# Kernel tuning notes

Hardware: AMD Instinct MI355X
Metric: run time of the kernel (lower is better)

## Reference

```python
import jax, jax.numpy as jnp
import numpy as np

B, S, D = 4, 2048, 1024
H, DK, DV = 16, 64, 64


def setup_inputs() -> dict:
    key = jax.random.key(0)
    ks = jax.random.split(key, 12)
    scale = 1.0 / np.sqrt(D)
    queries = jax.random.normal(ks[0], (B, S, D), dtype=jnp.float32)
    keys_ = jax.random.normal(ks[1], (B, S, D), dtype=jnp.float32)
    values = jax.random.normal(ks[2], (B, S, D), dtype=jnp.float32)
    # binary additive mask (1 = masked out), broadcastable over batch and heads
    mask = jax.random.randint(ks[3], (1, 1, S, S), 0, 2).astype(jnp.float32)
    Wq = jax.random.normal(ks[4], (D, H * DK), dtype=jnp.float32) * scale
    bq = jnp.zeros((H * DK,), dtype=jnp.float32)
    Wk = jax.random.normal(ks[5], (D, H * DK), dtype=jnp.float32) * scale
    bk = jnp.zeros((H * DK,), dtype=jnp.float32)
    Wv = jax.random.normal(ks[6], (D, H * DV), dtype=jnp.float32) * scale
    bv = jnp.zeros((H * DV,), dtype=jnp.float32)
    Wo = jax.random.normal(ks[7], (H * DV, D), dtype=jnp.float32) * scale
    bo = jnp.zeros((D,), dtype=jnp.float32)
    return {"queries": queries, "keys": keys_, "values": values, "mask": mask,
            "Wq": Wq, "bq": bq, "Wk": Wk, "bk": bk, "Wv": Wv, "bv": bv,
            "Wo": Wo, "bo": bo}


def reference(queries, keys, values, mask, Wq, bq, Wk, bk, Wv, bv, Wo, bo):
    b = queries.shape[0]
    # projections + split heads: [B, S, H*Dh] -> [B, H, S, Dh]
    q = (queries @ Wq + bq).reshape(b, -1, H, DK).transpose(0, 2, 1, 3)
    k = (keys @ Wk + bk).reshape(b, -1, H, DK).transpose(0, 2, 1, 3)
    v = (values @ Wv + bv).reshape(b, -1, H, DV).transpose(0, 2, 1, 3)
    scores = jnp.einsum("bhqd,bhkd->bhqk", q, k) / jnp.sqrt(jnp.float32(DK))
    scores = scores + mask * (-1e9)
    attn = jax.nn.softmax(scores, axis=-1)
    ctx = jnp.einsum("bhqk,bhkd->bhqd", attn, v)  # [B, H, S, DV]
    ctx = ctx.transpose(0, 2, 1, 3).reshape(b, -1, H * DV)
    return ctx @ Wo + bo
```

## Files before the change

### kernel.cpp

```cpp
#include <hip/hip_runtime.h>
#include <cstdint>
#include <cstddef>

typedef __attribute__((ext_vector_type(8))) short bf16x8;
typedef __attribute__((ext_vector_type(4))) short bf16x4;
typedef __attribute__((ext_vector_type(4))) float f32x4;

__device__ __forceinline__ unsigned short f2bf(float f) {
    union { float f; unsigned int u; } v; v.f = f;
    unsigned int r = v.u + 0x7FFFu + ((v.u >> 16) & 1u);
    return (unsigned short)(r >> 16);
}
__device__ __forceinline__ unsigned int pk2(float a, float b) {
    return (unsigned int)f2bf(a) | ((unsigned int)f2bf(b) << 16);
}
__device__ __forceinline__ unsigned int pkfast(float a, float b) {
    unsigned int ua = __builtin_bit_cast(unsigned int, a) + 0x8000u;
    unsigned int ub = __builtin_bit_cast(unsigned int, b) + 0x8000u;
    return __builtin_amdgcn_perm(ub, ua, 0x07060302u);
}

typedef __attribute__((address_space(1))) void gvoid;
typedef __attribute__((address_space(3))) void svoid;
__device__ __forceinline__ void ld16_lds(const void* g, void* l) {
    __builtin_amdgcn_global_load_lds((gvoid*)g, (svoid*)l, 16, 0, 0);
}

#define QSCALE 0.1803368801111204f

__global__ __launch_bounds__(256)
void cvt_bf16(const float* __restrict__ A, const float* __restrict__ B,
              const float* __restrict__ C,
              unsigned short* __restrict__ oa, unsigned short* __restrict__ ob,
              unsigned short* __restrict__ oc)
{
    const float* src = (blockIdx.y == 0) ? A : (blockIdx.y == 1) ? B : C;
    unsigned short* dst = (blockIdx.y == 0) ? oa : (blockIdx.y == 1) ? ob : oc;
    const size_t i = ((size_t)blockIdx.x * 256 + threadIdx.x) * 8;
    float4 a = *(const float4*)(src + i);
    float4 b = *(const float4*)(src + i + 4);
    uint4 p;
    p.x = pk2(a.x, a.y); p.y = pk2(a.z, a.w);
    p.z = pk2(b.x, b.y); p.w = pk2(b.z, b.w);
    *(uint4*)(dst + i) = p;
}

__global__ __launch_bounds__(256)
void prep_weights(const float* __restrict__ W0, const float* __restrict__ W1,
                  const float* __restrict__ W2, const float* __restrict__ W3,
                  unsigned short* __restrict__ T0, unsigned short* __restrict__ T1,
                  unsigned short* __restrict__ T2, unsigned short* __restrict__ T3)
{
    __shared__ float t[32][33];
    const int z = blockIdx.z;
    const float* W = (z == 0) ? W0 : (z == 1) ? W1 : (z == 2) ? W2 : W3;
    unsigned short* Wt = (z == 0) ? T0 : (z == 1) ? T1 : (z == 2) ? T2 : T3;
    const int n0 = blockIdx.x * 32, k0 = blockIdx.y * 32;
    const int tx = threadIdx.x & 31, ty = threadIdx.x >> 5;
#pragma unroll
    for (int i = 0; i < 4; i++)
        t[ty + 8 * i][tx] = W[(size_t)(k0 + ty + 8 * i) * 1024 + n0 + tx];
    __syncthreads();
#pragma unroll
    for (int i = 0; i < 4; i++)
        Wt[(size_t)(n0 + ty + 8 * i) * 1024 + k0 + tx] = f2bf(t[tx][ty + 8 * i]);
}

__global__ __launch_bounds__(256)
void mask_pack(const float* __restrict__ m, unsigned char* __restrict__ bits)
{
    const size_t i = ((size_t)blockIdx.x * 256 + threadIdx.x) * 8;
    float4 a = *(const float4*)(m + i);
    float4 b = *(const float4*)(m + i + 4);
    unsigned c = 0;
    c |= (a.x != 0.f) ? 1u : 0u;
    c |= (a.y != 0.f) ? 2u : 0u;
    c |= (a.z != 0.f) ? 4u : 0u;
    c |= (a.w != 0.f) ? 8u : 0u;
    c |= (b.x != 0.f) ? 16u : 0u;
    c |= (b.y != 0.f) ? 32u : 0u;
    c |= (b.z != 0.f) ? 64u : 0u;
    c |= (b.w != 0.f) ? 128u : 0u;
    bits[i >> 3] = (unsigned char)c;
}

__global__ __launch_bounds__(256, 3)
void qkv_gemm(const unsigned short* __restrict__ A0,
              const unsigned short* __restrict__ W0,
              const float* __restrict__ bq, const float* __restrict__ bk,
              const float* __restrict__ bv,
              unsigned short* __restrict__ out0)
{
    __shared__ __align__(16) unsigned short sm[18432];

    const int z = blockIdx.z;
    const unsigned short* A  = A0 + ((size_t)z << 23);
    const unsigned short* Wt = W0 + ((size_t)z << 20);
    const float* bias = (z == 0) ? bq : (z == 1) ? bk : bv;
    unsigned short* ob = out0 + ((size_t)z << 23);

    const int tid = threadIdx.x, lane = tid & 63, wave = tid >> 6;
    const int quad = lane >> 4, l16 = lane & 15;
    const int wr = wave >> 1, wc = wave & 1;
    const int m0 = blockIdx.x * 128, n0 = blockIdx.y * 128;

    const char* Ab = (const char*)A  + (size_t)m0 * 2048;
    const char* Bb = (const char*)Wt + (size_t)n0 * 2048;
    const int sr0 = tid >> 2, sc0 = (tid & 3) << 4;

    f32x4 acc[4][4];
#pragma unroll
    for (int i = 0; i < 4; i++)
#pragma unroll
        for (int j = 0; j < 4; j++) acc[i][j] = (f32x4){0.f, 0.f, 0.f, 0.f};

    {
        char* Ad = (char*)sm;
        char* Bd = Ad + 8192;
        ld16_lds(Ab + (size_t)sr0 * 2048 + sc0,        Ad + tid * 16);
        ld16_lds(Ab + (size_t)(sr0 + 64) * 2048 + sc0, Ad + (256 + tid) * 16);
        ld16_lds(Bb + (size_t)sr0 * 2048 + sc0,        Bd + tid * 16);
        ld16_lds(Bb + (size_t)(sr0 + 64) * 2048 + sc0, Bd + (256 + tid) * 16);
    }

    for (int it = 0; it < 32; ++it) {
        const int cur = it & 1;
        __syncthreads();
        if (it < 31) {
            const int kb2 = (it + 1) * 64;
            char* Ad = (char*)(sm + (cur ^ 1) * 8192);
            char* Bd = Ad + 8192;
            ld16_lds(Ab + (size_t)sr0 * 2048 + kb2 + sc0,        Ad + tid * 16);
            ld16_lds(Ab + (size_t)(sr0 + 64) * 2048 + kb2 + sc0, Ad + (256 + tid) * 16);
            ld16_lds(Bb + (size_t)sr0 * 2048 + kb2 + sc0,        Bd + tid * 16);
            ld16_lds(Bb + (size_t)(sr0 + 64) * 2048 + kb2 + sc0, Bd + (256 + tid) * 16);
        }
        const unsigned short* As = sm + cur * 8192;
        const unsigned short* Bs = As + 4096;

        bf16x8 af[4], bfr[4];
#pragma unroll
        for (int mt = 0; mt < 4; mt++)
            af[mt] = *(const bf16x8*)&As[(wr * 64 + mt * 16 + l16) * 32 + quad * 8];
#pragma unroll
        for (int nt = 0; nt < 4; nt++)
            bfr[nt] = *(const bf16x8*)&Bs[(wc * 64 + nt * 16 + l16) * 32 + quad * 8];
#pragma unroll
        for (int mt = 0; mt < 4; mt++)
#pragma unroll
            for (int nt = 0; nt < 4; nt++)
                acc[mt][nt] = __builtin_amdgcn_mfma_f32_16x16x32_bf16(af[mt], bfr[nt], acc[mt][nt], 0, 0, 0);
    }

    float bvv[4];
#pragma unroll
    for (int nt = 0; nt < 4; nt++) bvv[nt] = bias[n0 + wc * 64 + nt * 16 + l16];

    if (z < 2) {
#pragma unroll
        for (int mt = 0; mt < 4; mt++) {
            const int m = m0 + wr * 64 + mt * 16 + quad * 4;
            const int b = m >> 11;
#pragma unroll
            for (int nt = 0; nt < 4; nt++) {
                const int n = n0 + wc * 64 + nt * 16 + l16;
                const int h = n >> 6, dk = n & 63;
#pragma unroll
                for (int r = 0; r < 4; r++) {
                    const int s = (m + r) & 2047;
                    float o = acc[mt][nt][r] + bvv[nt];
                    if (z == 0) o *= QSCALE;
                    ob[((size_t)((b << 4) + h) * 2048 + s) * 64 + dk] = f2bf(o);
                }
            }
        }
    } else {
        __syncthreads();
        unsigned short* T = sm + wave * (64 * 72);
#pragma unroll
        for (int mt = 0; mt < 4; mt++)
#pragma unroll
            for (int nt = 0; nt < 4; nt++)
#pragma unroll
                for (int r = 0; r < 4; r++)
                    T[(nt * 16 + l16) * 72 + mt * 16 + quad * 4 + r] = f2bf(acc[mt][nt][r] + bvv[nt]);
        __syncthreads();
#pragma unroll
        for (int i = 0; i < 8; i++) {
            const int nl = i * 8 + (lane >> 3);
            const int mc = lane & 7;
            uint4 v = *(const uint4*)&T[nl * 72 + mc * 8];
            const int n  = n0 + wc * 64 + nl;
            const int mg = m0 + wr * 64 + mc * 8;
            const int b = mg >> 11, s = mg & 2047;
            const int h = n >> 6, dv = n & 63;
            *(uint4*)&ob[((size_t)((b << 4) + h) * 64 + dv) * 2048 + s] = v;
        }
    }
}

__global__ __launch_bounds__(256, 3)
void gemm_final(const unsigned short* __restrict__ A,
                const unsigned short* __restrict__ Wt, const float* __restrict__ bias,
                float* __restrict__ of)
{
    __shared__ __align__(16) unsigned short sm[16384];

    const int tid = threadIdx.x, lane = tid & 63, wave = tid >> 6;
    const int quad = lane >> 4, l16 = lane & 15;
    const int wr = wave >> 1, wc = wave & 1;
    const int m0 = blockIdx.x * 128, n0 = blockIdx.y * 128;

    const char* Ab = (const char*)A  + (size_t)m0 * 2048;
    const char* Bb = (const char*)Wt + (size_t)n0 * 2048;
    const int sr0 = tid >> 2, sc0 = (tid & 3) << 4;

    f32x4 acc[4][4];
#pragma unroll
    for (int i = 0; i < 4; i++)
#pragma unroll
        for (int j = 0; j < 4; j++) acc[i][j] = (f32x4){0.f, 0.f, 0.f, 0.f};

    {
        char* Ad = (char*)sm;
        char* Bd = Ad + 8192;
        ld16_lds(Ab + (size_t)sr0 * 2048 + sc0,        Ad + tid * 16);
        ld16_lds(Ab + (size_t)(sr0 + 64) * 2048 + sc0, Ad + (256 + tid) * 16);
        ld16_lds(Bb + (size_t)sr0 * 2048 + sc0,        Bd + tid * 16);
        ld16_lds(Bb + (size_t)(sr0 + 64) * 2048 + sc0, Bd + (256 + tid) * 16);
    }

    for (int it = 0; it < 32; ++it) {
        const int cur = it & 1;
        __syncthreads();
        if (it < 31) {
            const int kb2 = (it + 1) * 64;
            char* Ad = (char*)(sm + (cur ^ 1) * 8192);
            char* Bd = Ad + 8192;
            ld16_lds(Ab + (size_t)sr0 * 2048 + kb2 + sc0,        Ad + tid * 16);
            ld16_lds(Ab + (size_t)(sr0 + 64) * 2048 + kb2 + sc0, Ad + (256 + tid) * 16);
            ld16_lds(Bb + (size_t)sr0 * 2048 + kb2 + sc0,        Bd + tid * 16);
            ld16_lds(Bb + (size_t)(sr0 + 64) * 2048 + kb2 + sc0, Bd + (256 + tid) * 16);
        }
        const unsigned short* As = sm + cur * 8192;
        const unsigned short* Bs = As + 4096;

        bf16x8 af[4], bfr[4];
#pragma unroll
        for (int mt = 0; mt < 4; mt++)
            af[mt] = *(const bf16x8*)&As[(wr * 64 + mt * 16 + l16) * 32 + quad * 8];
#pragma unroll
        for (int nt = 0; nt < 4; nt++)
            bfr[nt] = *(const bf16x8*)&Bs[(wc * 64 + nt * 16 + l16) * 32 + quad * 8];
#pragma unroll
        for (int mt = 0; mt < 4; mt++)
#pragma unroll
            for (int nt = 0; nt < 4; nt++)
                acc[mt][nt] = __builtin_amdgcn_mfma_f32_16x16x32_bf16(af[mt], bfr[nt], acc[mt][nt], 0, 0, 0);
    }

    float bvv[4];
#pragma unroll
    for (int nt = 0; nt < 4; nt++) bvv[nt] = bias[n0 + wc * 64 + nt * 16 + l16];
#pragma unroll
    for (int mt = 0; mt < 4; mt++) {
        const int m = m0 + wr * 64 + mt * 16 + quad * 4;
#pragma unroll
        for (int nt = 0; nt < 4; nt++) {
            const int n = n0 + wc * 64 + nt * 16 + l16;
#pragma unroll
            for (int r = 0; r < 4; r++)
                of[(size_t)(m + r) * 1024 + n] = acc[mt][nt][r] + bvv[nt];
        }
    }
}

__global__ __launch_bounds__(256, 4)
void attn_kernel(const unsigned short* __restrict__ q,
                 const unsigned short* __restrict__ k,
                 const unsigned short* __restrict__ vT,
                 const unsigned int* __restrict__ mbits,
                 unsigned short* __restrict__ ctx)
{
    __shared__ __align__(16) unsigned short Ks[2][64 * 64];
    __shared__ __align__(16) unsigned short Vs[2][64 * 64];

    const int tid = threadIdx.x, lane = tid & 63, wave = tid >> 6;
    const int quad = lane >> 4, l16 = lane & 15;
    const int sw = l16 & 7;
    const int bid = blockIdx.x;
    const int qblk = bid & 15, h = (bid >> 4) & 15, b = bid >> 8;

    const unsigned short* qb = q  + (size_t)(b * 16 + h) * 2048 * 64;
    const unsigned short* kb = k  + (size_t)(b * 16 + h) * 2048 * 64;
    const unsigned short* vb = vT + (size_t)(b * 16 + h) * 64 * 2048;

    const int c0 = tid, c1 = 256 + tid;
    const int r0 = c0 >> 3, gcc0 = (c0 & 7) ^ (r0 & 7);
    const int r1 = c1 >> 3, gcc1 = (c1 & 7) ^ (r1 & 7);

    int qrow[2];
    bf16x8 qf[2][2];
    f32x4 O0[4], O1[4];
    float l_i[2] = {0.f, 0.f};
#pragma unroll
    for (int g = 0; g < 2; g++) {
        qrow[g] = qblk * 128 + wave * 32 + g * 16 + l16;
        qf[g][0] = *(const bf16x8*)&qb[qrow[g] * 64 + quad * 8];
        qf[g][1] = *(const bf16x8*)&qb[qrow[g] * 64 + 32 + quad * 8];
    }
#pragma unroll
    for (int i = 0; i < 4; i++) { O0[i] = (f32x4){0.f,0.f,0.f,0.f}; O1[i] = (f32x4){0.f,0.f,0.f,0.f}; }
    const unsigned int* mrow0 = mbits + (size_t)qrow[0] * 64;
    const unsigned int* mrow1 = mbits + (size_t)qrow[1] * 64;

    {
        ld16_lds((const char*)kb + (size_t)r0 * 128 + gcc0 * 16, (char*)Ks[0] + c0 * 16);
        ld16_lds((const char*)kb + (size_t)r1 * 128 + gcc1 * 16, (char*)Ks[0] + c1 * 16);
        ld16_lds((const char*)vb + (size_t)r0 * 4096 + gcc0 * 16, (char*)Vs[0] + c0 * 16);
        ld16_lds((const char*)vb + (size_t)r1 * 4096 + gcc1 * 16, (char*)Vs[0] + c1 * 16);
    }
    uint2 mwc0 = *(const uint2*)&mrow0[0];
    uint2 mwc1 = *(const uint2*)&mrow1[0];

    for (int it = 0; it < 32; ++it) {
        const int kt = it << 6;
        const int cur = it & 1, nxt = cur ^ 1;
        __syncthreads();

        if (it < 31) {
            const char* kg = (const char*)kb + (size_t)(kt + 64) * 128;
            const char* vg = (const char*)vb + (size_t)(kt + 64) * 2;
            ld16_lds(kg + (size_t)r0 * 128 + gcc0 * 16, (char*)Ks[nxt] + c0 * 16);
            ld16_lds(kg + (size_t)r1 * 128 + gcc1 * 16, (char*)Ks[nxt] + c1 * 16);
            ld16_lds(vg + (size_t)r0 * 4096 + gcc0 * 16, (char*)Vs[nxt] + c0 * 16);
            ld16_lds(vg + (size_t)r1 * 4096 + gcc1 * 16, (char*)Vs[nxt] + c1 * 16);
        }
        const int mi = (it < 31) ? ((kt + 64) >> 5) : 0;
        uint2 mwn0 = *(const uint2*)&mrow0[mi];
        uint2 mwn1 = *(const uint2*)&mrow1[mi];

        const unsigned short* Kc = Ks[cur];
        const unsigned short* Vc = Vs[cur];

        f32x4 S0[4], S1[4];
#pragma unroll
        for (int mt = 0; mt < 4; mt++) {
            const unsigned short* kp = Kc + (mt * 16 + l16) * 64;
            bf16x8 ka0 = *(const bf16x8*)&kp[((quad    ) ^ sw) * 8];
            bf16x8 ka1 = *(const bf16x8*)&kp[((4 + quad) ^ sw) * 8];
            f32x4 z0 = (f32x4){0.f,0.f,0.f,0.f};
            f32x4 z1 = (f32x4){0.f,0.f,0.f,0.f};
            z0 = __builtin_amdgcn_mfma_f32_16x16x32_bf16(ka0, qf[0][0], z0, 0, 0, 0);
            S0[mt] = __builtin_amdgcn_mfma_f32_16x16x32_bf16(ka1, qf[0][1], z0, 0, 0, 0);
            z1 = __builtin_amdgcn_mfma_f32_16x16x32_bf16(ka0, qf[1][0], z1, 0, 0, 0);
            S1[mt] = __builtin_amdgcn_mfma_f32_16x16x32_bf16(ka1, qf[1][1], z1, 0, 0, 0);
        }
        float sum0 = 0.f, sum1 = 0.f;
        bf16x4 pf0[4], pf1[4];
#pragma unroll
        for (int mt = 0; mt < 4; mt++) {
            const unsigned int wm0 = ((mt & 2) ? mwc0.y : mwc0.x) >> (((mt & 1) << 4) + (quad << 2));
            const unsigned int wm1 = ((mt & 2) ? mwc1.y : mwc1.x) >> (((mt & 1) << 4) + (quad << 2));
#pragma unroll
            for (int r = 0; r < 4; r++) {
                float s0 = ((wm0 >> r) & 1u) ? -1e8f : S0[mt][r];
                float s1 = ((wm1 >> r) & 1u) ? -1e8f : S1[mt][r];
                s0 = __builtin_amdgcn_exp2f(s0);
                s1 = __builtin_amdgcn_exp2f(s1);
                S0[mt][r] = s0; sum0 += s0;
                S1[mt][r] = s1; sum1 += s1;
            }
            uint2 u0, u1;
            u0.x = pkfast(S0[mt][0], S0[mt][1]); u0.y = pkfast(S0[mt][2], S0[mt][3]);
            u1.x = pkfast(S1[mt][0], S1[mt][1]); u1.y = pkfast(S1[mt][2], S1[mt][3]);
            pf0[mt] = __builtin_bit_cast(bf16x4, u0);
            pf1[mt] = __builtin_bit_cast(bf16x4, u1);
        }
        l_i[0] += sum0; l_i[1] += sum1;

#pragma unroll
        for (int dvt = 0; dvt < 4; dvt++) {
            const unsigned short* vp = Vc + (dvt * 16 + l16) * 64;
#pragma unroll
            for (int mt = 0; mt < 4; mt++) {
                uint2 vv = *(const uint2*)&vp[((2 * mt + (quad >> 1)) ^ sw) * 8 + (quad & 1) * 4];
                bf16x4 va = __builtin_bit_cast(bf16x4, vv);
                O0[dvt] = __builtin_amdgcn_mfma_f32_16x16x16bf16_1k(va, pf0[mt], O0[dvt], 0, 0, 0);
                O1[dvt] = __builtin_amdgcn_mfma_f32_16x16x16bf16_1k(va, pf1[mt], O1[dvt], 0, 0, 0);
            }
        }
        mwc0 = mwn0; mwc1 = mwn1;
    }
#pragma unroll
    for (int g = 0; g < 2; g++) {
        float lsum = l_i[g];
        lsum += __shfl_xor(lsum, 16);
        lsum += __shfl_xor(lsum, 32);
        const float rl = __builtin_amdgcn_rcpf(lsum);
        const f32x4* O = g ? O1 : O0;
#pragma unroll
        for (int dvt = 0; dvt < 4; dvt++) {
            uint2 st;
            st.x = pk2(O[dvt][0] * rl, O[dvt][1] * rl);
            st.y = pk2(O[dvt][2] * rl, O[dvt][3] * rl);
            *(uint2*)&ctx[(size_t)(b * 2048 + qrow[g]) * 1024 + h * 64 + dvt * 16 + quad * 4] = st;
        }
    }
}

extern "C" void kernel_launch(void* const* d_in, const int* in_sizes, int n_in,
                              void* d_out, int out_size, void* d_ws, size_t ws_size,
                              hipStream_t stream)
{
    const float* Qin = (const float*)d_in[0];
    const float* Kin = (const float*)d_in[1];
    const float* Vin = (const float*)d_in[2];
    const float* Msk = (const float*)d_in[3];
    const float* Wq  = (const float*)d_in[4];
    const float* bq  = (const float*)d_in[5];
    const float* Wk  = (const float*)d_in[6];
    const float* bk  = (const float*)d_in[7];
    const float* Wv  = (const float*)d_in[8];
    const float* bv  = (const float*)d_in[9];
    const float* Wo  = (const float*)d_in[10];
    const float* bo  = (const float*)d_in[11];

    unsigned short* w = (unsigned short*)d_ws;
    unsigned short* wtq  = w;
    unsigned short* wtk  = w + (1u << 20);
    unsigned short* wtv  = w + 2u * (1u << 20);
    unsigned short* wto  = w + 3u * (1u << 20);
    unsigned short* qcv  = w + 4u * (1u << 20);
    unsigned short* kcv  = qcv + (1u << 23);
    unsigned short* vcv  = kcv + (1u << 23);
    unsigned short* qb   = vcv + (1u << 23);
    unsigned short* kb   = qb  + (1u << 23);
    unsigned short* vTb  = kb  + (1u << 23);
    unsigned short* ctxb = qcv;
    unsigned long long* mb = (unsigned long long*)(vTb + (1u << 23));

    prep_weights<<<dim3(32, 32, 4), 256, 0, stream>>>(Wq, Wk, Wv, Wo, wtq, wtk, wtv, wto);
    mask_pack<<<2048, 256, 0, stream>>>(Msk, (unsigned char*)mb);
    cvt_bf16<<<dim3(4096, 3), 256, 0, stream>>>(Qin, Kin, Vin, qcv, kcv, vcv);
    qkv_gemm<<<dim3(64, 8, 3), 256, 0, stream>>>(qcv, wtq, bq, bk, bv, qb);
    attn_kernel<<<1024, 256, 0, stream>>>(qb, kb, vTb, (const unsigned int*)mb, ctxb);
    gemm_final<<<dim3(64, 8), 256, 0, stream>>>(ctxb, wto, bo, (float*)d_out);
}
```

Baseline: 388.0 us.

## Merge preprocessing kernels, compute softmax denominator via MFMA, use native bf16 pack

The three preprocessing kernels (activation conversion, mask bit-packing, weight transpose) become one launch that dispatches on block index, removing two kernel launches. In the attention kernel the per-row softmax sum is now an MFMA against a ones vector instead of scalar adds plus cross-lane shuffles. The P packing uses the hardware bf16 pack instruction when available. The qkv_gemm launch bounds rise to 4 blocks per CU. The sum is now taken over the bf16-rounded probabilities, and the higher occupancy target may limit registers.

```diff
diff --git a/kernel.cpp b/kernel.cpp
--- a/kernel.cpp
+++ b/kernel.cpp
@@ -14,10 +14,15 @@
 __device__ __forceinline__ unsigned int pk2(float a, float b) {
     return (unsigned int)f2bf(a) | ((unsigned int)f2bf(b) << 16);
 }
-__device__ __forceinline__ unsigned int pkfast(float a, float b) {
+__device__ __forceinline__ unsigned int pkpair(float a, float b) {
+#if __has_builtin(__builtin_amdgcn_cvt_pk_bf16_f32)
+    auto r = __builtin_amdgcn_cvt_pk_bf16_f32(a, b);
+    return __builtin_bit_cast(unsigned int, r);
+#else
     unsigned int ua = __builtin_bit_cast(unsigned int, a) + 0x8000u;
     unsigned int ub = __builtin_bit_cast(unsigned int, b) + 0x8000u;
     return __builtin_amdgcn_perm(ub, ua, 0x07060302u);
+#endif
 }
 
 typedef __attribute__((address_space(1))) void gvoid;
@@ -29,62 +34,58 @@
 #define QSCALE 0.1803368801111204f
 
 __global__ __launch_bounds__(256)
-void cvt_bf16(const float* __restrict__ A, const float* __restrict__ B,
-              const float* __restrict__ C,
-              unsigned short* __restrict__ oa, unsigned short* __restrict__ ob,
-              unsigned short* __restrict__ oc)
-{
-    const float* src = (blockIdx.y == 0) ? A : (blockIdx.y == 1) ? B : C;
-    unsigned short* dst = (blockIdx.y == 0) ? oa : (blockIdx.y == 1) ? ob : oc;
-    const size_t i = ((size_t)blockIdx.x * 256 + threadIdx.x) * 8;
-    float4 a = *(const float4*)(src + i);
-    float4 b = *(const float4*)(src + i + 4);
-    uint4 p;
-    p.x = pk2(a.x, a.y); p.y = pk2(a.z, a.w);
-    p.z = pk2(b.x, b.y); p.w = pk2(b.z, b.w);
-    *(uint4*)(dst + i) = p;
-}
-
-__global__ __launch_bounds__(256)
-void prep_weights(const float* __restrict__ W0, const float* __restrict__ W1,
-                  const float* __restrict__ W2, const float* __restrict__ W3,
-                  unsigned short* __restrict__ T0, unsigned short* __restrict__ T1,
-                  unsigned short* __restrict__ T2, unsigned short* __restrict__ T3)
+void preprocess(const float* __restrict__ Qin, const float* __restrict__ Kin,
+                const float* __restrict__ Vin, const float* __restrict__ Msk,
+                const float* __restrict__ Wq, const float* __restrict__ Wk,
+                const float* __restrict__ Wv, const float* __restrict__ Wo,
+                unsigned short* __restrict__ acts, unsigned char* __restrict__ mbits,
+                unsigned short* __restrict__ wts)
 {
     __shared__ float t[32][33];
-    const int z = blockIdx.z;
-    const float* W = (z == 0) ? W0 : (z == 1) ? W1 : (z == 2) ? W2 : W3;
-    unsigned short* Wt = (z == 0) ? T0 : (z == 1) ? T1 : (z == 2) ? T2 : T3;
-    const int n0 = blockIdx.x * 32, k0 = blockIdx.y * 32;
-    const int tx = threadIdx.x & 31, ty = threadIdx.x >> 5;
-#pragma unroll
-    for (int i = 0; i < 4; i++)
-        t[ty + 8 * i][tx] = W[(size_t)(k0 + ty + 8 * i) * 1024 + n0 + tx];
-    __syncthreads();
-#pragma unroll
-    for (int i = 0; i < 4; i++)
-        Wt[(size_t)(n0 + ty + 8 * i) * 1024 + k0 + tx] = f2bf(t[tx][ty + 8 * i]);
-}
-
-__global__ __launch_bounds__(256)
-void mask_pack(const float* __restrict__ m, unsigned char* __restrict__ bits)
-{
-    const size_t i = ((size_t)blockIdx.x * 256 + threadIdx.x) * 8;
-    float4 a = *(const float4*)(m + i);
-    float4 b = *(const float4*)(m + i + 4);
-    unsigned c = 0;
-    c |= (a.x != 0.f) ? 1u : 0u;
-    c |= (a.y != 0.f) ? 2u : 0u;
-    c |= (a.z != 0.f) ? 4u : 0u;
-    c |= (a.w != 0.f) ? 8u : 0u;
-    c |= (b.x != 0.f) ? 16u : 0u;
-    c |= (b.y != 0.f) ? 32u : 0u;
-    c |= (b.z != 0.f) ? 64u : 0u;
-    c |= (b.w != 0.f) ? 128u : 0u;
-    bits[i >> 3] = (unsigned char)c;
-}
-
-__global__ __launch_bounds__(256, 3)
+    const int bx = blockIdx.x, tid = threadIdx.x;
+    if (bx < 12288) {
+        const int which = bx >> 12;
+        const float* src = (which == 0) ? Qin : (which == 1) ? Kin : Vin;
+        unsigned short* dst = acts + ((size_t)which << 23);
+        const size_t i = ((size_t)(bx & 4095) * 256 + tid) * 8;
+        float4 a = *(const float4*)(src + i);
+        float4 b = *(const float4*)(src + i + 4);
+        uint4 p;
+        p.x = pk2(a.x, a.y); p.y = pk2(a.z, a.w);
+        p.z = pk2(b.x, b.y); p.w = pk2(b.z, b.w);
+        *(uint4*)(dst + i) = p;
+    } else if (bx < 14336) {
+        const size_t i = ((size_t)(bx - 12288) * 256 + tid) * 8;
+        float4 a = *(const float4*)(Msk + i);
+        float4 b = *(const float4*)(Msk + i + 4);
+        unsigned c = 0;
+        c |= (a.x != 0.f) ? 1u : 0u;
+        c |= (a.y != 0.f) ? 2u : 0u;
+        c |= (a.z != 0.f) ? 4u : 0u;
+        c |= (a.w != 0.f) ? 8u : 0u;
+        c |= (b.x != 0.f) ? 16u : 0u;
+        c |= (b.y != 0.f) ? 32u : 0u;
+        c |= (b.z != 0.f) ? 64u : 0u;
+        c |= (b.w != 0.f) ? 128u : 0u;
+        mbits[i >> 3] = (unsigned char)c;
+    } else {
+        const int idx = bx - 14336;
+        const int z = idx >> 10, rem = idx & 1023;
+        const float* W = (z == 0) ? Wq : (z == 1) ? Wk : (z == 2) ? Wv : Wo;
+        unsigned short* Wt = wts + ((size_t)z << 20);
+        const int n0 = (rem & 31) << 5, k0 = (rem >> 5) << 5;
+        const int tx = tid & 31, ty = tid >> 5;
+#pragma unroll
+        for (int i = 0; i < 4; i++)
+            t[ty + 8 * i][tx] = W[(size_t)(k0 + ty + 8 * i) * 1024 + n0 + tx];
+        __syncthreads();
+#pragma unroll
+        for (int i = 0; i < 4; i++)
+            Wt[(size_t)(n0 + ty + 8 * i) * 1024 + k0 + tx] = f2bf(t[tx][ty + 8 * i]);
+    }
+}
+
+__global__ __launch_bounds__(256, 4)
 void qkv_gemm(const unsigned short* __restrict__ A0,
               const unsigned short* __restrict__ W0,
               const float* __restrict__ bq, const float* __restrict__ bk,
@@ -302,7 +303,8 @@
     int qrow[2];
     bf16x8 qf[2][2];
     f32x4 O0[4], O1[4];
-    float l_i[2] = {0.f, 0.f};
+    f32x4 lacc0 = (f32x4){0.f,0.f,0.f,0.f}, lacc1 = (f32x4){0.f,0.f,0.f,0.f};
+    const bf16x4 vones = (bf16x4){(short)0x3F80, (short)0x3F80, (short)0x3F80, (short)0x3F80};
 #pragma unroll
     for (int g = 0; g < 2; g++) {
         qrow[g] = qblk * 128 + wave * 32 + g * 16 + l16;
@@ -356,29 +358,28 @@
             z1 = __builtin_amdgcn_mfma_f32_16x16x32_bf16(ka0, qf[1][0], z1, 0, 0, 0);
             S1[mt] = __builtin_amdgcn_mfma_f32_16x16x32_bf16(ka1, qf[1][1], z1, 0, 0, 0);
         }
-        float sum0 = 0.f, sum1 = 0.f;
         bf16x4 pf0[4], pf1[4];
 #pragma unroll
         for (int mt = 0; mt < 4; mt++) {
             const unsigned int wm0 = ((mt & 2) ? mwc0.y : mwc0.x) >> (((mt & 1) << 4) + (quad << 2));
             const unsigned int wm1 = ((mt & 2) ? mwc1.y : mwc1.x) >> (((mt & 1) << 4) + (quad << 2));
+            float p0[4], p1[4];
 #pragma unroll
             for (int r = 0; r < 4; r++) {
-                float s0 = ((wm0 >> r) & 1u) ? -1e8f : S0[mt][r];
-                float s1 = ((wm1 >> r) & 1u) ? -1e8f : S1[mt][r];
-                s0 = __builtin_amdgcn_exp2f(s0);
-                s1 = __builtin_amdgcn_exp2f(s1);
-                S0[mt][r] = s0; sum0 += s0;
-                S1[mt][r] = s1; sum1 += s1;
+                p0[r] = __builtin_amdgcn_exp2f(((wm0 >> r) & 1u) ? -1e8f : S0[mt][r]);
+                p1[r] = __builtin_amdgcn_exp2f(((wm1 >> r) & 1u) ? -1e8f : S1[mt][r]);
             }
             uint2 u0, u1;
-            u0.x = pkfast(S0[mt][0], S0[mt][1]); u0.y = pkfast(S0[mt][2], S0[mt][3]);
-            u1.x = pkfast(S1[mt][0], S1[mt][1]); u1.y = pkfast(S1[mt][2], S1[mt][3]);
+            u0.x = pkpair(p0[0], p0[1]); u0.y = pkpair(p0[2], p0[3]);
+            u1.x = pkpair(p1[0], p1[1]); u1.y = pkpair(p1[2], p1[3]);
             pf0[mt] = __builtin_bit_cast(bf16x4, u0);
             pf1[mt] = __builtin_bit_cast(bf16x4, u1);
         }
-        l_i[0] += sum0; l_i[1] += sum1;
-
+#pragma unroll
+        for (int mt = 0; mt < 4; mt++) {
+            lacc0 = __builtin_amdgcn_mfma_f32_16x16x16bf16_1k(vones, pf0[mt], lacc0, 0, 0, 0);
+            lacc1 = __builtin_amdgcn_mfma_f32_16x16x16bf16_1k(vones, pf1[mt], lacc1, 0, 0, 0);
+        }
 #pragma unroll
         for (int dvt = 0; dvt < 4; dvt++) {
             const unsigned short* vp = Vc + (dvt * 16 + l16) * 64;
@@ -394,10 +395,7 @@
     }
 #pragma unroll
     for (int g = 0; g < 2; g++) {
-        float lsum = l_i[g];
-        lsum += __shfl_xor(lsum, 16);
-        lsum += __shfl_xor(lsum, 32);
-        const float rl = __builtin_amdgcn_rcpf(lsum);
+        const float rl = __builtin_amdgcn_rcpf(g ? lacc1[0] : lacc0[0]);
         const f32x4* O = g ? O1 : O0;
 #pragma unroll
         for (int dvt = 0; dvt < 4; dvt++) {
@@ -427,23 +425,18 @@
     const float* bo  = (const float*)d_in[11];
 
     unsigned short* w = (unsigned short*)d_ws;
-    unsigned short* wtq  = w;
-    unsigned short* wtk  = w + (1u << 20);
-    unsigned short* wtv  = w + 2u * (1u << 20);
+    unsigned short* wts  = w;
     unsigned short* wto  = w + 3u * (1u << 20);
     unsigned short* qcv  = w + 4u * (1u << 20);
-    unsigned short* kcv  = qcv + (1u << 23);
-    unsigned short* vcv  = kcv + (1u << 23);
-    unsigned short* qb   = vcv + (1u << 23);
+    unsigned short* qb   = qcv + 3u * (1u << 23);
     unsigned short* kb   = qb  + (1u << 23);
     unsigned short* vTb  = kb  + (1u << 23);
     unsigned short* ctxb = qcv;
     unsigned long long* mb = (unsigned long long*)(vTb + (1u << 23));
 
-    prep_weights<<<dim3(32, 32, 4), 256, 0, stream>>>(Wq, Wk, Wv, Wo, wtq, wtk, wtv, wto);
-    mask_pack<<<2048, 256, 0, stream>>>(Msk, (unsigned char*)mb);
-    cvt_bf16<<<dim3(4096, 3), 256, 0, stream>>>(Qin, Kin, Vin, qcv, kcv, vcv);
-    qkv_gemm<<<dim3(64, 8, 3), 256, 0, stream>>>(qcv, wtq, bq, bk, bv, qb);
+    preprocess<<<18432, 256, 0, stream>>>(Qin, Kin, Vin, Msk, Wq, Wk, Wv, Wo,
+                                          qcv, (unsigned char*)mb, wts);
+    qkv_gemm<<<dim3(64, 8, 3), 256, 0, stream>>>(qcv, wts, bq, bk, bv, qb);
     attn_kernel<<<1024, 256, 0, stream>>>(qb, kb, vTb, (const unsigned int*)mb, ctxb);
     gemm_final<<<dim3(64, 8), 256, 0, stream>>>(ctxb, wto, bo, (float*)d_out);
 }
```

Result: faster. 376.9 us (-2.9%).
